# Kernel tuning notes

Hardware: AMD Instinct MI355X
Metric: run time of the kernel (lower is better)

## Reference

```python
import jax, jax.numpy as jnp
import numpy as np

N_CUST, N_ART, E, H = 1_000_000, 100_000, 2_000_000, 128

def setup_inputs() -> dict:
    key = jax.random.key(0)
    ks = jax.random.split(key, 6)
    return {
        "z_customer": jax.random.normal(ks[0], (N_CUST, H), dtype=jnp.float32),
        "z_article": jax.random.normal(ks[1], (N_ART, H), dtype=jnp.float32),
        "row": jax.random.randint(ks[2], (E,), 0, N_CUST, dtype=jnp.int64),
        "col": jax.random.randint(ks[3], (E,), 0, N_ART, dtype=jnp.int64),
        "W1": jax.random.normal(ks[4], (2 * H, H), dtype=jnp.float32) * (1.0 / np.sqrt(2 * H)),
        "b1": jnp.zeros((H,), dtype=jnp.float32),
        "W2": jax.random.normal(ks[5], (H, 1), dtype=jnp.float32) * (1.0 / np.sqrt(H)),
        "b2": jnp.zeros((1,), dtype=jnp.float32),
    }

def reference(z_customer, z_article, row, col, W1, b1, W2, b2):
    # gather node embeddings for each labeled edge and concat: [E, 2H]
    z = jnp.concatenate([z_customer[row], z_article[col]], axis=-1)
    h = jax.nn.relu(z @ W1 + b1)          # [E, H]
    out = h @ W2 + b2                      # [E, 1]
    return out.reshape(-1)                 # [E]
```

## Files before the change

kernel.cpp:

```cpp
#include <hip/hip_runtime.h>

typedef short short8 __attribute__((ext_vector_type(8)));
typedef float f32x4 __attribute__((ext_vector_type(4)));
typedef unsigned int uint4v __attribute__((ext_vector_type(4)));

static constexpr int kH = 128;

__device__ __forceinline__ unsigned f2bf(float f) {
    unsigned u = __builtin_bit_cast(unsigned, f);
    u += 0x7fffu + ((u >> 16) & 1u);
    return u >> 16;
}
__device__ __forceinline__ unsigned pack_bf16x2(float a, float b) {
    return f2bf(a) | (f2bf(b) << 16);
}

struct U128 { unsigned x, y, z, w; };

__global__ __launch_bounds__(256, 2) void edge_mlp(
    const float* __restrict__ zc, const float* __restrict__ za,
    const int* __restrict__ row, const int* __restrict__ col,
    const float* __restrict__ W1, const float* __restrict__ b1,
    const float* __restrict__ W2, const float* __restrict__ b2,
    float* __restrict__ out, int E, int ntiles)
{
    __shared__ unsigned ldsB[16384];

    const int tid = threadIdx.x;

    #pragma unroll 4
    for (int i = 0; i < 64; ++i) {
        int lin2 = tid + i * 256;
        int j  = (lin2 & 3) * 2;
        int l  = (lin2 >> 2) & 63;
        int nt = (lin2 >> 8) & 7;
        int s  = (lin2 >> 11) & 7;
        int q = l >> 4, n = l & 15;
        int k = s * 32 + q * 8 + j;
        int ncol = nt * 16 + n;
        float f0 = W1[k * kH + ncol];
        float f1 = W1[(k + 1) * kH + ncol];
        ldsB[lin2] = pack_bf16x2(f0, f1);
    }
    __syncthreads();

    const int w   = tid >> 6;
    const int l   = tid & 63;
    const int q   = l >> 4;
    const int n16 = l & 15;

    float b1v[8], w2v[8];
    #pragma unroll
    for (int nt = 0; nt < 8; ++nt) {
        b1v[nt] = b1[nt * 16 + n16];
        w2v[nt] = W2[nt * 16 + n16];
    }
    const float b2s = b2[0];

    for (int tile = blockIdx.x; tile < ntiles; tile += gridDim.x) {
        const int ebase = tile * 128 + w * 32;
        int e0 = ebase + n16;
        int e1 = ebase + 16 + n16;
        int ce0 = min(e0, E - 1);
        int ce1 = min(e1, E - 1);
        const float* pc0 = zc + (size_t)row[ce0] * kH;
        const float* pa0 = za + (size_t)col[ce0] * kH;
        const float* pc1 = zc + (size_t)row[ce1] * kH;
        const float* pa1 = za + (size_t)col[ce1] * kH;

        f32x4 acc[2][8];
        #pragma unroll
        for (int mt = 0; mt < 2; ++mt)
            #pragma unroll
            for (int nt = 0; nt < 8; ++nt)
                acc[mt][nt] = f32x4{0.f, 0.f, 0.f, 0.f};

        #pragma unroll
        for (int s = 0; s < 8; ++s) {
            const float* s0 = (s < 4) ? (pc0 + s * 32) : (pa0 + (s - 4) * 32);
            const float* s1 = (s < 4) ? (pc1 + s * 32) : (pa1 + (s - 4) * 32);
            float4 fa = *(const float4*)(s0 + q * 8);
            float4 fb = *(const float4*)(s0 + q * 8 + 4);
            float4 fc = *(const float4*)(s1 + q * 8);
            float4 fd = *(const float4*)(s1 + q * 8 + 4);
            U128 ua{pack_bf16x2(fa.x, fa.y), pack_bf16x2(fa.z, fa.w),
                    pack_bf16x2(fb.x, fb.y), pack_bf16x2(fb.z, fb.w)};
            U128 ub{pack_bf16x2(fc.x, fc.y), pack_bf16x2(fc.z, fc.w),
                    pack_bf16x2(fd.x, fd.y), pack_bf16x2(fd.z, fd.w)};
            short8 a0 = __builtin_bit_cast(short8, ua);
            short8 a1 = __builtin_bit_cast(short8, ub);
            #pragma unroll
            for (int nt = 0; nt < 8; ++nt) {
                uint4v bu = *(const uint4v*)(&ldsB[((s * 8 + nt) * 64 + l) * 4]);
                short8 bv = __builtin_bit_cast(short8, bu);
                acc[0][nt] = __builtin_amdgcn_mfma_f32_16x16x32_bf16(a0, bv, acc[0][nt], 0, 0, 0);
                acc[1][nt] = __builtin_amdgcn_mfma_f32_16x16x32_bf16(a1, bv, acc[1][nt], 0, 0, 0);
            }
        }

        #pragma unroll
        for (int mt = 0; mt < 2; ++mt) {
            float p[4];
            #pragma unroll
            for (int r = 0; r < 4; ++r) {
                float sum = 0.f;
                #pragma unroll
                for (int nt = 0; nt < 8; ++nt)
                    sum += fmaxf(acc[mt][nt][r] + b1v[nt], 0.f) * w2v[nt];
                sum += __shfl_xor(sum, 1);
                sum += __shfl_xor(sum, 2);
                sum += __shfl_xor(sum, 4);
                sum += __shfl_xor(sum, 8);
                p[r] = sum + b2s;
            }
            if (n16 == 0) {
                int eb = ebase + mt * 16 + q * 4;
                if (eb + 3 < E) {
                    *(float4*)(out + eb) = make_float4(p[0], p[1], p[2], p[3]);
                } else {
                    #pragma unroll
                    for (int r = 0; r < 4; ++r)
                        if (eb + r < E) out[eb + r] = p[r];
                }
            }
        }
    }
}

extern "C" void kernel_launch(void* const* d_in, const int* in_sizes, int n_in,
                              void* d_out, int out_size, void* d_ws, size_t ws_size,
                              hipStream_t stream) {
    const float* zc = (const float*)d_in[0];
    const float* za = (const float*)d_in[1];
    const int*   row = (const int*)d_in[2];
    const int*   col = (const int*)d_in[3];
    const float* W1 = (const float*)d_in[4];
    const float* b1 = (const float*)d_in[5];
    const float* W2 = (const float*)d_in[6];
    const float* b2 = (const float*)d_in[7];
    float* out = (float*)d_out;

    int E = in_sizes[2];
    int ntiles = (E + 127) / 128;
    int grid = ntiles < 1024 ? ntiles : 1024;
    edge_mlp<<<grid, 256, 0, stream>>>(zc, za, row, col, W1, b1, W2, b2, out, E, ntiles);
}
```

Before: 1.452 ms.

## Pre-convert embedding tables to bf16 in workspace before gather MLP

```diff
diff --git a/kernel.cpp b/kernel.cpp
--- a/kernel.cpp
+++ b/kernel.cpp
@@ -17,7 +17,122 @@
 
 struct U128 { unsigned x, y, z, w; };
 
-__global__ __launch_bounds__(256, 2) void edge_mlp(
+__global__ void cvt_bf16(const float* __restrict__ src, unsigned* __restrict__ dst, long n4) {
+    long i = (long)blockIdx.x * blockDim.x + threadIdx.x;
+    if (i < n4) {
+        float4 f = ((const float4*)src)[i];
+        ((uint2*)dst)[i] = make_uint2(pack_bf16x2(f.x, f.y), pack_bf16x2(f.z, f.w));
+    }
+}
+
+template <int BLK>
+__device__ __forceinline__ void fill_w1(const float* __restrict__ W1, unsigned* ldsB, int tid) {
+    #pragma unroll 4
+    for (int i = 0; i < 16384 / BLK; ++i) {
+        int lin2 = tid + i * BLK;
+        int j  = (lin2 & 3) * 2;
+        int l  = (lin2 >> 2) & 63;
+        int nt = (lin2 >> 8) & 7;
+        int s  = (lin2 >> 11) & 7;
+        int q = l >> 4, n = l & 15;
+        int k = s * 32 + q * 8 + j;
+        int ncol = nt * 16 + n;
+        ldsB[lin2] = pack_bf16x2(W1[k * kH + ncol], W1[(k + 1) * kH + ncol]);
+    }
+}
+
+__device__ __forceinline__ void epilogue(
+    const f32x4 acc[2][8], const float b1v[8], const float w2v[8], float b2s,
+    float* __restrict__ out, int ebase, int E, int q, int n16)
+{
+    #pragma unroll
+    for (int mt = 0; mt < 2; ++mt) {
+        float p[4];
+        #pragma unroll
+        for (int r = 0; r < 4; ++r) {
+            float sum = 0.f;
+            #pragma unroll
+            for (int nt = 0; nt < 8; ++nt)
+                sum += fmaxf(acc[mt][nt][r] + b1v[nt], 0.f) * w2v[nt];
+            sum += __shfl_xor(sum, 1);
+            sum += __shfl_xor(sum, 2);
+            sum += __shfl_xor(sum, 4);
+            sum += __shfl_xor(sum, 8);
+            p[r] = sum + b2s;
+        }
+        if (n16 == 0) {
+            int eb = ebase + mt * 16 + q * 4;
+            if (eb + 3 < E) {
+                *(float4*)(out + eb) = make_float4(p[0], p[1], p[2], p[3]);
+            } else {
+                #pragma unroll
+                for (int r = 0; r < 4; ++r)
+                    if (eb + r < E) out[eb + r] = p[r];
+            }
+        }
+    }
+}
+
+__global__ __launch_bounds__(512, 4) void edge_mlp_bf16(
+    const unsigned short* __restrict__ zc, const unsigned short* __restrict__ za,
+    const int* __restrict__ row, const int* __restrict__ col,
+    const float* __restrict__ W1, const float* __restrict__ b1,
+    const float* __restrict__ W2, const float* __restrict__ b2,
+    float* __restrict__ out, int E, int ntiles)
+{
+    __shared__ unsigned ldsB[16384];
+    const int tid = threadIdx.x;
+    fill_w1<512>(W1, ldsB, tid);
+    __syncthreads();
+
+    const int w   = tid >> 6;
+    const int l   = tid & 63;
+    const int q   = l >> 4;
+    const int n16 = l & 15;
+
+    float b1v[8], w2v[8];
+    #pragma unroll
+    for (int nt = 0; nt < 8; ++nt) {
+        b1v[nt] = b1[nt * 16 + n16];
+        w2v[nt] = W2[nt * 16 + n16];
+    }
+    const float b2s = b2[0];
+
+    for (int tile = blockIdx.x; tile < ntiles; tile += gridDim.x) {
+        const int ebase = tile * 256 + w * 32;
+        int ce0 = min(ebase + n16, E - 1);
+        int ce1 = min(ebase + 16 + n16, E - 1);
+        const unsigned short* pc0 = zc + (size_t)row[ce0] * kH;
+        const unsigned short* pa0 = za + (size_t)col[ce0] * kH;
+        const unsigned short* pc1 = zc + (size_t)row[ce1] * kH;
+        const unsigned short* pa1 = za + (size_t)col[ce1] * kH;
+
+        f32x4 acc[2][8];
+        #pragma unroll
+        for (int mt = 0; mt < 2; ++mt)
+            #pragma unroll
+            for (int nt = 0; nt < 8; ++nt)
+                acc[mt][nt] = f32x4{0.f, 0.f, 0.f, 0.f};
+
+        #pragma unroll
+        for (int s = 0; s < 8; ++s) {
+            const unsigned short* s0 = (s < 4) ? (pc0 + s * 32) : (pa0 + (s - 4) * 32);
+            const unsigned short* s1 = (s < 4) ? (pc1 + s * 32) : (pa1 + (s - 4) * 32);
+            short8 a0 = *(const short8*)(s0 + q * 8);
+            short8 a1 = *(const short8*)(s1 + q * 8);
+            #pragma unroll
+            for (int nt = 0; nt < 8; ++nt) {
+                uint4v bu = *(const uint4v*)(&ldsB[((s * 8 + nt) * 64 + l) * 4]);
+                short8 bv = __builtin_bit_cast(short8, bu);
+                acc[0][nt] = __builtin_amdgcn_mfma_f32_16x16x32_bf16(a0, bv, acc[0][nt], 0, 0, 0);
+                acc[1][nt] = __builtin_amdgcn_mfma_f32_16x16x32_bf16(a1, bv, acc[1][nt], 0, 0, 0);
+            }
+        }
+        epilogue(acc, b1v, w2v, b2s, out, ebase, E, q, n16);
+    }
+}
+
+__global__ __launch_bounds__(512, 4) void edge_mlp_f32(
     const float* __restrict__ zc, const float* __restrict__ za,
     const int* __restrict__ row, const int* __restrict__ col,
     const float* __restrict__ W1, const float* __restrict__ b1,
@@ -25,23 +140,8 @@
     float* __restrict__ out, int E, int ntiles)
 {
     __shared__ unsigned ldsB[16384];
-
     const int tid = threadIdx.x;
-
-    #pragma unroll 4
-    for (int i = 0; i < 64; ++i) {
-        int lin2 = tid + i * 256;
-        int j  = (lin2 & 3) * 2;
-        int l  = (lin2 >> 2) & 63;
-        int nt = (lin2 >> 8) & 7;
-        int s  = (lin2 >> 11) & 7;
-        int q = l >> 4, n = l & 15;
-        int k = s * 32 + q * 8 + j;
-        int ncol = nt * 16 + n;
-        float f0 = W1[k * kH + ncol];
-        float f1 = W1[(k + 1) * kH + ncol];
-        ldsB[lin2] = pack_bf16x2(f0, f1);
-    }
+    fill_w1<512>(W1, ldsB, tid);
     __syncthreads();
 
     const int w   = tid >> 6;
@@ -58,11 +158,9 @@
     const float b2s = b2[0];
 
     for (int tile = blockIdx.x; tile < ntiles; tile += gridDim.x) {
-        const int ebase = tile * 128 + w * 32;
-        int e0 = ebase + n16;
-        int e1 = ebase + 16 + n16;
-        int ce0 = min(e0, E - 1);
-        int ce1 = min(e1, E - 1);
+        const int ebase = tile * 256 + w * 32;
+        int ce0 = min(ebase + n16, E - 1);
+        int ce1 = min(ebase + 16 + n16, E - 1);
         const float* pc0 = zc + (size_t)row[ce0] * kH;
         const float* pa0 = za + (size_t)col[ce0] * kH;
         const float* pc1 = zc + (size_t)row[ce1] * kH;
@@ -97,33 +195,7 @@
                 acc[1][nt] = __builtin_amdgcn_mfma_f32_16x16x32_bf16(a1, bv, acc[1][nt], 0, 0, 0);
             }
         }
-
-        #pragma unroll
-        for (int mt = 0; mt < 2; ++mt) {
-            float p[4];
-            #pragma unroll
-            for (int r = 0; r < 4; ++r) {
-                float sum = 0.f;
-                #pragma unroll
-                for (int nt = 0; nt < 8; ++nt)
-                    sum += fmaxf(acc[mt][nt][r] + b1v[nt], 0.f) * w2v[nt];
-                sum += __shfl_xor(sum, 1);
-                sum += __shfl_xor(sum, 2);
-                sum += __shfl_xor(sum, 4);
-                sum += __shfl_xor(sum, 8);
-                p[r] = sum + b2s;
-            }
-            if (n16 == 0) {
-                int eb = ebase + mt * 16 + q * 4;
-                if (eb + 3 < E) {
-                    *(float4*)(out + eb) = make_float4(p[0], p[1], p[2], p[3]);
-                } else {
-                    #pragma unroll
-                    for (int r = 0; r < 4; ++r)
-                        if (eb + r < E) out[eb + r] = p[r];
-                }
-            }
-        }
+        epilogue(acc, b1v, w2v, b2s, out, ebase, E, q, n16);
     }
 }
 
@@ -141,7 +213,21 @@
     float* out = (float*)d_out;
 
     int E = in_sizes[2];
-    int ntiles = (E + 127) / 128;
-    int grid = ntiles < 1024 ? ntiles : 1024;
-    edge_mlp<<<grid, 256, 0, stream>>>(zc, za, row, col, W1, b1, W2, b2, out, E, ntiles);
-}
+    long nc_elems = in_sizes[0];
+    long na_elems = in_sizes[1];
+    size_t need = (size_t)(nc_elems + na_elems) * 2;
+
+    int ntiles = (E + 255) / 256;
+    int grid = ntiles < 512 ? ntiles : 512;
+
+    if (ws_size >= need) {
+        unsigned short* wsC = (unsigned short*)d_ws;
+        unsigned short* wsA = wsC + nc_elems;
+        long c4 = nc_elems / 4, a4 = na_elems / 4;
+        cvt_bf16<<<(int)((c4 + 255) / 256), 256, 0, stream>>>(zc, (unsigned*)wsC, c4);
+        cvt_bf16<<<(int)((a4 + 255) / 256), 256, 0, stream>>>(za, (unsigned*)wsA, a4);
+        edge_mlp_bf16<<<grid, 512, 0, stream>>>(wsC, wsA, row, col, W1, b1, W2, b2, out, E, ntiles);
+    } else {
+        edge_mlp_f32<<<grid, 512, 0, stream>>>(zc, za, row, col, W1, b1, W2, b2, out, E, ntiles);
+    }
+}
```

Result: slower. 1.784 ms (+22.9%).

## Use 512-thread blocks with one M-tile per wave and software-prefetched gathers

Applied to the files above, without the earlier changes.

```diff
diff --git a/kernel.cpp b/kernel.cpp
--- a/kernel.cpp
+++ b/kernel.cpp
@@ -17,7 +17,23 @@
 
 struct U128 { unsigned x, y, z, w; };
 
-__global__ __launch_bounds__(256, 2) void edge_mlp(
+template <int BLK>
+__device__ __forceinline__ void fill_w1(const float* __restrict__ W1, unsigned* ldsB, int tid) {
+    #pragma unroll 4
+    for (int i = 0; i < 16384 / BLK; ++i) {
+        int lin2 = tid + i * BLK;
+        int j  = (lin2 & 3) * 2;
+        int l  = (lin2 >> 2) & 63;
+        int nt = (lin2 >> 8) & 7;
+        int s  = (lin2 >> 11) & 7;
+        int q = l >> 4, n = l & 15;
+        int k = s * 32 + q * 8 + j;
+        int ncol = nt * 16 + n;
+        ldsB[lin2] = pack_bf16x2(W1[k * kH + ncol], W1[(k + 1) * kH + ncol]);
+    }
+}
+
+__global__ __launch_bounds__(512, 4) void edge_mlp_f32(
     const float* __restrict__ zc, const float* __restrict__ za,
     const int* __restrict__ row, const int* __restrict__ col,
     const float* __restrict__ W1, const float* __restrict__ b1,
@@ -25,23 +41,8 @@
     float* __restrict__ out, int E, int ntiles)
 {
     __shared__ unsigned ldsB[16384];
-
     const int tid = threadIdx.x;
-
-    #pragma unroll 4
-    for (int i = 0; i < 64; ++i) {
-        int lin2 = tid + i * 256;
-        int j  = (lin2 & 3) * 2;
-        int l  = (lin2 >> 2) & 63;
-        int nt = (lin2 >> 8) & 7;
-        int s  = (lin2 >> 11) & 7;
-        int q = l >> 4, n = l & 15;
-        int k = s * 32 + q * 8 + j;
-        int ncol = nt * 16 + n;
-        float f0 = W1[k * kH + ncol];
-        float f1 = W1[(k + 1) * kH + ncol];
-        ldsB[lin2] = pack_bf16x2(f0, f1);
-    }
+    fill_w1<512>(W1, ldsB, tid);
     __syncthreads();
 
     const int w   = tid >> 6;
@@ -56,74 +57,75 @@
         w2v[nt] = W2[nt * 16 + n16];
     }
     const float b2s = b2[0];
+    const int stride = gridDim.x;
 
-    for (int tile = blockIdx.x; tile < ntiles; tile += gridDim.x) {
-        const int ebase = tile * 128 + w * 32;
-        int e0 = ebase + n16;
-        int e1 = ebase + 16 + n16;
-        int ce0 = min(e0, E - 1);
-        int ce1 = min(e1, E - 1);
-        const float* pc0 = zc + (size_t)row[ce0] * kH;
-        const float* pa0 = za + (size_t)col[ce0] * kH;
-        const float* pc1 = zc + (size_t)row[ce1] * kH;
-        const float* pa1 = za + (size_t)col[ce1] * kH;
+    int tile = blockIdx.x;
+    if (tile >= ntiles) return;
 
-        f32x4 acc[2][8];
+    int ce = min(tile * 128 + w * 16 + n16, E - 1);
+    int r0 = row[ce], c0 = col[ce];
+
+    for (; tile < ntiles; tile += stride) {
+        const float* pc = zc + (size_t)r0 * kH;
+        const float* pa = za + (size_t)c0 * kH;
+
+        int ntile = tile + stride;
+        int nce = min(min(ntile, ntiles - 1) * 128 + w * 16 + n16, E - 1);
+        int nr = row[nce], nc = col[nce];
+
+        float4 P[4][2];
+        auto ld = [&](int d, int s) {
+            const float* sp = (s < 4) ? (pc + s * 32) : (pa + (s - 4) * 32);
+            P[d][0] = *(const float4*)(sp + q * 8);
+            P[d][1] = *(const float4*)(sp + q * 8 + 4);
+        };
+        ld(0, 0); ld(1, 1); ld(2, 2); ld(3, 3);
+
+        f32x4 acc[8];
         #pragma unroll
-        for (int mt = 0; mt < 2; ++mt)
-            #pragma unroll
-            for (int nt = 0; nt < 8; ++nt)
-                acc[mt][nt] = f32x4{0.f, 0.f, 0.f, 0.f};
+        for (int nt = 0; nt < 8; ++nt) acc[nt] = f32x4{0.f, 0.f, 0.f, 0.f};
 
         #pragma unroll
         for (int s = 0; s < 8; ++s) {
-            const float* s0 = (s < 4) ? (pc0 + s * 32) : (pa0 + (s - 4) * 32);
-            const float* s1 = (s < 4) ? (pc1 + s * 32) : (pa1 + (s - 4) * 32);
-            float4 fa = *(const float4*)(s0 + q * 8);
-            float4 fb = *(const float4*)(s0 + q * 8 + 4);
-            float4 fc = *(const float4*)(s1 + q * 8);
-            float4 fd = *(const float4*)(s1 + q * 8 + 4);
+            const int d = s & 3;
+            float4 fa = P[d][0], fb = P[d][1];
             U128 ua{pack_bf16x2(fa.x, fa.y), pack_bf16x2(fa.z, fa.w),
                     pack_bf16x2(fb.x, fb.y), pack_bf16x2(fb.z, fb.w)};
-            U128 ub{pack_bf16x2(fc.x, fc.y), pack_bf16x2(fc.z, fc.w),
-                    pack_bf16x2(fd.x, fd.y), pack_bf16x2(fd.z, fd.w)};
             short8 a0 = __builtin_bit_cast(short8, ua);
-            short8 a1 = __builtin_bit_cast(short8, ub);
+            if (s < 4) ld(d, s + 4);
             #pragma unroll
             for (int nt = 0; nt < 8; ++nt) {
                 uint4v bu = *(const uint4v*)(&ldsB[((s * 8 + nt) * 64 + l) * 4]);
                 short8 bv = __builtin_bit_cast(short8, bu);
-                acc[0][nt] = __builtin_amdgcn_mfma_f32_16x16x32_bf16(a0, bv, acc[0][nt], 0, 0, 0);
-                acc[1][nt] = __builtin_amdgcn_mfma_f32_16x16x32_bf16(a1, bv, acc[1][nt], 0, 0, 0);
+                acc[nt] = __builtin_amdgcn_mfma_f32_16x16x32_bf16(a0, bv, acc[nt], 0, 0, 0);
             }
         }
 
+        float p[4];
         #pragma unroll
-        for (int mt = 0; mt < 2; ++mt) {
-            float p[4];
+        for (int r = 0; r < 4; ++r) {
+            float sum = 0.f;
             #pragma unroll
-            for (int r = 0; r < 4; ++r) {
-                float sum = 0.f;
+            for (int nt = 0; nt < 8; ++nt)
+                sum += fmaxf(acc[nt][r] + b1v[nt], 0.f) * w2v[nt];
+            sum += __shfl_xor(sum, 1);
+            sum += __shfl_xor(sum, 2);
+            sum += __shfl_xor(sum, 4);
+            sum += __shfl_xor(sum, 8);
+            p[r] = sum + b2s;
+        }
+        if (n16 == 0) {
+            int eb = tile * 128 + w * 16 + q * 4;
+            if (eb + 3 < E) {
+                *(float4*)(out + eb) = make_float4(p[0], p[1], p[2], p[3]);
+            } else {
                 #pragma unroll
-                for (int nt = 0; nt < 8; ++nt)
-                    sum += fmaxf(acc[mt][nt][r] + b1v[nt], 0.f) * w2v[nt];
-                sum += __shfl_xor(sum, 1);
-                sum += __shfl_xor(sum, 2);
-                sum += __shfl_xor(sum, 4);
-                sum += __shfl_xor(sum, 8);
-                p[r] = sum + b2s;
-            }
-            if (n16 == 0) {
-                int eb = ebase + mt * 16 + q * 4;
-                if (eb + 3 < E) {
-                    *(float4*)(out + eb) = make_float4(p[0], p[1], p[2], p[3]);
-                } else {
-                    #pragma unroll
-                    for (int r = 0; r < 4; ++r)
-                        if (eb + r < E) out[eb + r] = p[r];
-                }
+                for (int r = 0; r < 4; ++r)
+                    if (eb + r < E) out[eb + r] = p[r];
             }
         }
+
+        r0 = nr; c0 = nc;
     }
 }
 
@@ -142,6 +144,7 @@
 
     int E = in_sizes[2];
     int ntiles = (E + 127) / 128;
-    int grid = ntiles < 1024 ? ntiles : 1024;
-    edge_mlp<<<grid, 256, 0, stream>>>(zc, za, row, col, W1, b1, W2, b2, out, E, ntiles);
+    int grid = ntiles < 512 ? ntiles : 512;
+
+    edge_mlp_f32<<<grid, 512, 0, stream>>>(zc, za, row, col, W1, b1, W2, b2, out, E, ntiles);
 }
```

After: 2.149 ms. 1.48x slower.
